# Kernel optimization log

Measured on AMD Instinct MI355X. Metric: run time of the kernel, lower is better.

The kernel has to match this reference:

```python
import jax, jax.numpy as jnp
import numpy as np

DEPTH, D, HEADS, PS, C_IN = 12, 1024, 8, 16, 1
B, H, W = 8, 512, 512


def setup_inputs() -> dict:
    key = jax.random.key(0)
    ks = jax.random.split(key, 8)
    s = 0.02
    rn = lambda k, shp: jax.random.normal(k, shp, jnp.float32) * s
    return dict(
        x=jax.random.normal(ks[0], (B, C_IN, H, W), jnp.float32),
        conv_w=rn(ks[1], (D, C_IN, PS, PS)),
        conv_b=jnp.zeros((D,), jnp.float32),
        ln1_g=jnp.ones((DEPTH, D), jnp.float32),
        ln1_b=jnp.zeros((DEPTH, D), jnp.float32),
        qkv_w=rn(ks[2], (DEPTH, 3 * D, D)),
        qkv_b=jnp.zeros((DEPTH, 3 * D), jnp.float32),
        proj_w=rn(ks[3], (DEPTH, D, D)),
        proj_b=jnp.zeros((DEPTH, D), jnp.float32),
        ln2_g=jnp.ones((DEPTH, D), jnp.float32),
        ln2_b=jnp.zeros((DEPTH, D), jnp.float32),
        fc1_w=rn(ks[4], (DEPTH, 2 * D, D)),
        fc1_b=jnp.zeros((DEPTH, 2 * D), jnp.float32),
        fc2_w=rn(ks[5], (DEPTH, D, 2 * D)),
        fc2_b=jnp.zeros((DEPTH, D), jnp.float32),
    )


def _layernorm(x, g, b, eps=1e-5):
    m = x.mean(-1, keepdims=True)
    v = ((x - m) ** 2).mean(-1, keepdims=True)
    return (x - m) * jax.lax.rsqrt(v + eps) * g + b


def _pos_encoding(n, d):
    # faithful to the source: angle = pos / 10000 ** (2*i/d) with i the EVEN index
    pos = jnp.arange(n, dtype=jnp.float32)[:, None]
    i_even = jnp.arange(0, d, 2, dtype=jnp.float32)
    ang = pos / (10000.0 ** (2.0 * i_even / d))
    return jnp.stack([jnp.sin(ang), jnp.cos(ang)], axis=-1).reshape(n, d)


def reference(x, conv_w, conv_b, ln1_g, ln1_b, qkv_w, qkv_b, proj_w, proj_b,
              ln2_g, ln2_b, fc1_w, fc1_b, fc2_w, fc2_b):
    b = x.shape[0]
    Hp, Wp = H // PS, W // PS
    n = Hp * Wp  # 1024 tokens
    hd = D // HEADS
    scale = float(hd) ** -0.5

    # patch embed: conv with stride == kernel  ==  per-patch matmul
    patches = x.reshape(b, C_IN, Hp, PS, Wp, PS).transpose(0, 2, 4, 1, 3, 5)
    patches = patches.reshape(b, n, C_IN * PS * PS)
    tok = patches @ conv_w.reshape(D, -1).T + conv_b
    tok = tok + _pos_encoding(n, D)

    def step(t, p):
        g1, b1, qw, qb, pw, pb, g2, b2, f1w, f1b, f2w, f2b = p
        h = _layernorm(t, g1, b1)
        qkv = (h @ qw.T + qb).reshape(b, n, 3, HEADS, hd).transpose(2, 0, 3, 1, 4)
        q, k, v = qkv[0], qkv[1], qkv[2]  # [b, heads, n, hd]
        att = jax.nn.softmax(jnp.einsum('bhqd,bhkd->bhqk', q, k) * scale, axis=-1)
        o = jnp.einsum('bhqk,bhkd->bhqd', att, v).transpose(0, 2, 1, 3).reshape(b, n, D)
        t = t + o @ pw.T + pb
        h = _layernorm(t, g2, b2)
        h = jax.nn.gelu(h @ f1w.T + f1b, approximate=False)
        t = t + h @ f2w.T + f2b
        return t, None

    tok, _ = jax.lax.scan(step, tok, (ln1_g, ln1_b, qkv_w, qkv_b, proj_w, proj_b,
                                      ln2_g, ln2_b, fc1_w, fc1_b, fc2_w, fc2_b))

    # reconstruction: tok -> (b, 4, ps*ps, Hp, Wp); scatter fina[:,:,i::ps,j::ps] = x[:,:,k]
    x4 = tok.reshape(b, n, D // 4, 4).transpose(0, 3, 2, 1).reshape(b, 4, PS, PS, Hp, Wp)
    fina = x4.transpose(0, 1, 4, 2, 5, 3).reshape(b, 4, H, W)  # fina[b,c,a*ps+i,bb*ps+j]
    # rearrange 'b (h w) p1 p2 -> b 1 (p1 h) (p2 w)' with h=w=2
    out = fina.reshape(b, 2, 2, H, W).transpose(0, 3, 1, 4, 2).reshape(b, 1, 2 * H, 2 * W)
    return out
```

## Files before the change

kernel.cpp:

```cpp
#include <hip/hip_runtime.h>
#include <hip/hip_bf16.h>
#include <stdint.h>

typedef unsigned short u16;
typedef __attribute__((ext_vector_type(8))) __bf16 bf16x8;
typedef __attribute__((ext_vector_type(4))) float  f32x4;

__device__ __forceinline__ float bf2f(u16 v) {
    union { unsigned int u; float f; } x; x.u = ((unsigned int)v) << 16; return x.f;
}
__device__ __forceinline__ u16 f2bf(float f) {
    union { float f; unsigned int u; } x; x.f = f;
    unsigned int u = x.u;
    unsigned int lsb = (u >> 16) & 1u;
    u += 0x7fffu + lsb;
    return (u16)(u >> 16);
}

#define GLDS16(gp, lp)                                                         \
    __builtin_amdgcn_global_load_lds(                                          \
        (const __attribute__((address_space(1))) void*)(gp),                   \
        (__attribute__((address_space(3))) void*)(lp), 16, 0, 0)

__global__ __launch_bounds__(256) void cvt_kernel(const float* __restrict__ src,
                                                  u16* __restrict__ dst, int n4)
{
    int gid = blockIdx.x * 256 + threadIdx.x;
    if (gid < n4) {
        float4 v = ((const float4*)src)[gid];
        ushort4 o;
        o.x = f2bf(v.x); o.y = f2bf(v.y); o.z = f2bf(v.z); o.w = f2bf(v.w);
        ((ushort4*)dst)[gid] = o;
    }
}

__global__ __launch_bounds__(256) void cvt4_kernel(
    const float* __restrict__ s0, const float* __restrict__ s1,
    const float* __restrict__ s2, const float* __restrict__ s3,
    u16* __restrict__ d0, u16* __restrict__ d1,
    u16* __restrict__ d2, u16* __restrict__ d3)
{
    int gid = blockIdx.x * 256 + threadIdx.x;
    const float* s; u16* d; int idx;
    if (gid < 786432)                { s = s0; d = d0; idx = gid; }
    else if (gid < 1048576)          { s = s1; d = d1; idx = gid - 786432; }
    else if (gid < 1572864)          { s = s2; d = d2; idx = gid - 1048576; }
    else                             { s = s3; d = d3; idx = gid - 1572864; }
    float4 v = ((const float4*)s)[idx];
    ushort4 o;
    o.x = f2bf(v.x); o.y = f2bf(v.y); o.z = f2bf(v.z); o.w = f2bf(v.w);
    ((ushort4*)d)[idx] = o;
}

__global__ __launch_bounds__(512, 2) void gemm8p(
    const u16* __restrict__ A, const u16* __restrict__ B,
    const float* __restrict__ bias, const float* __restrict__ res,
    void* __restrict__ Cout, int c_fp32,
    int K, int lda, int ldb, int ldc, int ldres, float scale, int act)
{
    __shared__ __align__(16) u16 As[4][128 * 32];
    __shared__ __align__(16) u16 Bs[4][256 * 32];

    int nt = K >> 5;

    int gx  = gridDim.x;
    int nwg = gx * gridDim.y;
    int bid = blockIdx.y * gx + blockIdx.x;
    int cpx = nwg >> 3;
    int swz = (bid & 7) * cpx + (bid >> 3);
    int m0 = (swz / gx) << 7;
    int n0 = (swz % gx) << 8;

    int t = threadIdx.x;
    int w = t >> 6, l = t & 63;
    int wm = w >> 2, wn = w & 3;
    int lg = l >> 4, lr = l & 15;

    int arow = t >> 2, aslot = t & 3;
    const u16* Ag  = A + (long long)(m0 + arow) * lda + ((aslot ^ ((arow >> 1) & 3)) << 3);
    const u16* Bg0 = B + (long long)(n0 + arow) * ldb + ((aslot ^ ((arow >> 1) & 3)) << 3);
    const u16* Bg1 = Bg0 + (long long)128 * ldb;

#define STAGE_A(tt)  GLDS16(Ag  + ((long long)(tt) << 5), &As[(tt) & 3][w << 9])
#define STAGE_B0(tt) GLDS16(Bg0 + ((long long)(tt) << 5), &Bs[(tt) & 3][w << 9])
#define STAGE_B1(tt) GLDS16(Bg1 + ((long long)(tt) << 5), &Bs[(tt) & 3][4096 + (w << 9)])

    int sx = lg ^ ((lr >> 1) & 3);
    const u16* Asr = &As[0][0] + (wm << 11) + (lr << 5) + (sx << 3);
    const u16* Bsr = &Bs[0][0] + (wn << 11) + (lr << 5) + (sx << 3);

    f32x4 acc[4][4];
#pragma unroll
    for (int i = 0; i < 4; i++)
#pragma unroll
        for (int j = 0; j < 4; j++)
            acc[i][j] = (f32x4){0.f, 0.f, 0.f, 0.f};

    STAGE_A(0); STAGE_B0(0); STAGE_B1(0);
    if (nt > 1) { STAGE_A(1); STAGE_B0(1); STAGE_B1(1); }
    if (nt > 2) { STAGE_A(2); STAGE_B0(2); STAGE_B1(2); }
    asm volatile("s_waitcnt vmcnt(6)" ::: "memory");
    __builtin_amdgcn_s_barrier();
    __builtin_amdgcn_sched_barrier(0);

    for (int tt = 0; tt < nt; ++tt) {
        int buf = tt & 3;
        const u16* Ab = Asr + (buf << 12);
        const u16* Bb = Bsr + (buf << 13);

        bf16x8 av[4], bv0[2];
#pragma unroll
        for (int i = 0; i < 4; i++) av[i]  = *(const bf16x8*)(Ab + i * 512);
#pragma unroll
        for (int j = 0; j < 2; j++) bv0[j] = *(const bf16x8*)(Bb + j * 512);
        if (tt + 3 < nt) { STAGE_A(tt + 3); STAGE_B0(tt + 3); }
        __builtin_amdgcn_s_barrier();
        __builtin_amdgcn_sched_barrier(0);
        __builtin_amdgcn_s_setprio(1);
#pragma unroll
        for (int j = 0; j < 2; j++)
#pragma unroll
            for (int i = 0; i < 4; i++)
                acc[i][j] = __builtin_amdgcn_mfma_f32_16x16x32_bf16(av[i], bv0[j], acc[i][j], 0, 0, 0);
        __builtin_amdgcn_s_setprio(0);
        __builtin_amdgcn_s_barrier();
        __builtin_amdgcn_sched_barrier(0);

        bf16x8 bv1[2];
#pragma unroll
        for (int j = 0; j < 2; j++) bv1[j] = *(const bf16x8*)(Bb + (2 + j) * 512);
        if (tt + 3 < nt) STAGE_B1(tt + 3);
        __builtin_amdgcn_s_barrier();
        __builtin_amdgcn_sched_barrier(0);
        __builtin_amdgcn_s_setprio(1);
#pragma unroll
        for (int j = 0; j < 2; j++)
#pragma unroll
            for (int i = 0; i < 4; i++)
                acc[i][2 + j] = __builtin_amdgcn_mfma_f32_16x16x32_bf16(av[i], bv1[j], acc[i][2 + j], 0, 0, 0);
        __builtin_amdgcn_s_setprio(0);
        if (tt < nt - 3)       asm volatile("s_waitcnt vmcnt(6)" ::: "memory");
        else if (tt == nt - 3) asm volatile("s_waitcnt vmcnt(3)" ::: "memory");
        else if (tt == nt - 2) asm volatile("s_waitcnt vmcnt(0)" ::: "memory");
        __builtin_amdgcn_s_barrier();
        __builtin_amdgcn_sched_barrier(0);
    }
#undef STAGE_A
#undef STAGE_B0
#undef STAGE_B1

    int rq = lg << 2;
#pragma unroll
    for (int j = 0; j < 4; j++) {
        int col = n0 + (wn << 6) + (j << 4) + lr;
        float bvv = bias ? bias[col] : 0.f;
#pragma unroll
        for (int i = 0; i < 4; i++) {
#pragma unroll
            for (int r = 0; r < 4; r++) {
                int row = m0 + (wm << 6) + (i << 4) + rq + r;
                float v = acc[i][j][r] * scale + bvv;
                if (act) v = 0.5f * v * (1.f + erff(v * 0.70710678118654752f));
                if (res) v += res[(long long)row * ldres + col];
                long long idx = (long long)row * ldc + col;
                if (c_fp32) ((float*)Cout)[idx] = v;
                else        ((u16*)Cout)[idx]  = f2bf(v);
            }
        }
    }
}

#define ASCALE 0.08838834764831845f

__global__ __launch_bounds__(256) void attn_kernel(
    const u16* __restrict__ qkv, const u16* __restrict__ vt,
    u16* __restrict__ out)
{
    __shared__ __align__(16) u16 Ks[64 * 128];
    __shared__ __align__(16) u16 Vs[128 * 64];
    __shared__ __align__(16) u16 Ps[4][32 * 72];

    int bh = blockIdx.y; int b = bh >> 3, hd = bh & 7;
    int q0 = blockIdx.x << 7;
    int t = threadIdx.x, w = t >> 6, l = t & 63;
    int lg = l >> 4, lr = l & 15;

    const u16* qp = qkv + ((long long)(b * 1024 + q0 + (w << 5) + lr)) * 3072
                        + hd * 128 + (lg << 3);
    bf16x8 qf[2][4];
#pragma unroll
    for (int rb = 0; rb < 2; rb++)
#pragma unroll
        for (int kf = 0; kf < 4; kf++)
            qf[rb][kf] = *(const bf16x8*)(qp + rb * 16 * 3072 + (kf << 5));

    const u16* kg = qkv + ((long long)(b * 1024)) * 3072 + 1024 + hd * 128;
    const u16* vg = vt + (long long)bh * 131072;
    u16* Pw = &Ps[w][0];

    f32x4 oa[2][8];
#pragma unroll
    for (int rb = 0; rb < 2; rb++)
#pragma unroll
        for (int db = 0; db < 8; db++)
            oa[rb][db] = (f32x4){0.f, 0.f, 0.f, 0.f};
    float m_run[2][4], l_run[2][4];
#pragma unroll
    for (int rb = 0; rb < 2; rb++)
#pragma unroll
        for (int r = 0; r < 4; r++) { m_run[rb][r] = -1e30f; l_run[rb][r] = 0.f; }

    for (int kv0 = 0; kv0 < 1024; kv0 += 64) {
#pragma unroll
        for (int i = 0; i < 4; i++) {
            int ck   = (((w << 2) + i) << 6) + l;
            int krow = ck >> 4;
            int kslot = (ck & 15) ^ (krow & 7);
            GLDS16(kg + (long long)(kv0 + krow) * 3072 + (kslot << 3),
                   Ks + (((w << 2) + i) << 9));
            int vd   = ck >> 3;
            int vslot = (ck & 7) ^ (vd & 7);
            GLDS16(vg + (long long)vd * 1024 + kv0 + (vslot << 3),
                   Vs + (((w << 2) + i) << 9));
        }
        __syncthreads();

        f32x4 s[2][4];
#pragma unroll
        for (int kb = 0; kb < 4; kb++) {
            s[0][kb] = (f32x4){0.f, 0.f, 0.f, 0.f};
            s[1][kb] = (f32x4){0.f, 0.f, 0.f, 0.f};
        }
#pragma unroll
        for (int kf = 0; kf < 4; kf++)
#pragma unroll
            for (int kb = 0; kb < 4; kb++) {
                bf16x8 bk = *(const bf16x8*)
                    &Ks[(((kb << 4) + lr) << 7) + (((((kf << 2) + lg)) ^ (lr & 7)) << 3)];
                s[0][kb] = __builtin_amdgcn_mfma_f32_16x16x32_bf16(qf[0][kf], bk, s[0][kb], 0, 0, 0);
                s[1][kb] = __builtin_amdgcn_mfma_f32_16x16x32_bf16(qf[1][kf], bk, s[1][kb], 0, 0, 0);
            }

#pragma unroll
        for (int rb = 0; rb < 2; rb++) {
            float mx[4], al[4], rs[4];
#pragma unroll
            for (int r = 0; r < 4; r++)
                mx[r] = fmaxf(fmaxf(s[rb][0][r], s[rb][1][r]),
                              fmaxf(s[rb][2][r], s[rb][3][r]));
#pragma unroll
            for (int mask = 1; mask < 16; mask <<= 1)
#pragma unroll
                for (int r = 0; r < 4; r++)
                    mx[r] = fmaxf(mx[r], __shfl_xor(mx[r], mask));
#pragma unroll
            for (int r = 0; r < 4; r++) {
                float mn = fmaxf(m_run[rb][r], mx[r] * ASCALE);
                al[r] = __expf(m_run[rb][r] - mn);
                m_run[rb][r] = mn;
                rs[r] = 0.f;
            }
#pragma unroll
            for (int kb = 0; kb < 4; kb++)
#pragma unroll
                for (int r = 0; r < 4; r++) {
                    float p = __expf(s[rb][kb][r] * ASCALE - m_run[rb][r]);
                    rs[r] += p;
                    Pw[((rb << 4) + (lg << 2) + r) * 72 + (kb << 4) + lr] = f2bf(p);
                }
#pragma unroll
            for (int mask = 1; mask < 16; mask <<= 1)
#pragma unroll
                for (int r = 0; r < 4; r++)
                    rs[r] += __shfl_xor(rs[r], mask);
#pragma unroll
            for (int r = 0; r < 4; r++)
                l_run[rb][r] = l_run[rb][r] * al[r] + rs[r];
#pragma unroll
            for (int db = 0; db < 8; db++)
#pragma unroll
                for (int r = 0; r < 4; r++)
                    oa[rb][db][r] *= al[r];
        }

#pragma unroll
        for (int ks = 0; ks < 2; ks++) {
            bf16x8 pa0 = *(const bf16x8*)&Pw[lr * 72 + (ks << 5) + (lg << 3)];
            bf16x8 pa1 = *(const bf16x8*)&Pw[(16 + lr) * 72 + (ks << 5) + (lg << 3)];
#pragma unroll
            for (int db = 0; db < 8; db++) {
                bf16x8 vf = *(const bf16x8*)
                    &Vs[(((db << 4) + lr) << 6) + ((((ks << 2) + lg) ^ (lr & 7)) << 3)];
                oa[0][db] = __builtin_amdgcn_mfma_f32_16x16x32_bf16(pa0, vf, oa[0][db], 0, 0, 0);
                oa[1][db] = __builtin_amdgcn_mfma_f32_16x16x32_bf16(pa1, vf, oa[1][db], 0, 0, 0);
            }
        }
        __syncthreads();
    }

    long long obase = ((long long)(b * 1024 + q0 + (w << 5)) << 10) + hd * 128;
#pragma unroll
    for (int rb = 0; rb < 2; rb++) {
        float il[4];
#pragma unroll
        for (int r = 0; r < 4; r++) il[r] = 1.f / l_run[rb][r];
#pragma unroll
        for (int db = 0; db < 8; db++)
#pragma unroll
            for (int r = 0; r < 4; r++)
                out[obase + (long long)((rb << 4) + (lg << 2) + r) * 1024
                          + (db << 4) + lr] = f2bf(oa[rb][db][r] * il[r]);
    }
}

__global__ __launch_bounds__(256) void patches_kernel(const float* __restrict__ x,
                                                      u16* __restrict__ p)
{
    int gid = blockIdx.x * 256 + threadIdx.x;
    int c = gid & 255, tk = gid >> 8;
    int b = tk >> 10, n = tk & 1023;
    int ph = n >> 5, pw = n & 31;
    int i = c >> 4, j = c & 15;
    p[gid] = f2bf(x[((long long)b << 18) + (long long)(ph * 16 + i) * 512 + pw * 16 + j]);
}

__global__ __launch_bounds__(256) void posenc_kernel(float* __restrict__ tok)
{
    int gid = blockIdx.x * 256 + threadIdx.x;
    int d = gid & 1023;
    int n = (gid >> 10) & 1023;
    int j = d >> 1;
    float ang = (float)n * exp2f(-13.287712379549449f * (float)j * (1.0f / 256.0f));
    float pe = (d & 1) ? cosf(ang) : sinf(ang);
    tok[gid] += pe;
}

__global__ __launch_bounds__(256) void ln_kernel(const float* __restrict__ x,
                                                 const float* __restrict__ g,
                                                 const float* __restrict__ b,
                                                 u16* __restrict__ y)
{
    int row = blockIdx.x, t = threadIdx.x;
    const float* xr = x + (long long)row * 1024;
    float v[4]; float s = 0.f, ss = 0.f;
#pragma unroll
    for (int i = 0; i < 4; i++) { v[i] = xr[i * 256 + t]; s += v[i]; ss += v[i] * v[i]; }
    __shared__ float rs[256], rss[256];
    rs[t] = s; rss[t] = ss; __syncthreads();
    for (int o = 128; o > 0; o >>= 1) {
        if (t < o) { rs[t] += rs[t + o]; rss[t] += rss[t + o]; }
        __syncthreads();
    }
    float mean = rs[0] * (1.f / 1024.f);
    float var  = rss[0] * (1.f / 1024.f) - mean * mean;
    float rstd = rsqrtf(var + 1e-5f);
    u16* yr = y + (long long)row * 1024;
#pragma unroll
    for (int i = 0; i < 4; i++) {
        int d = i * 256 + t;
        yr[d] = f2bf((v[i] - mean) * rstd * g[d] + b[d]);
    }
}

__global__ __launch_bounds__(256) void vt_kernel(const u16* __restrict__ qkv,
                                                 u16* __restrict__ vt)
{
    int bh   = blockIdx.x >> 4;
    int tile = blockIdx.x & 15;
    int b = bh >> 3, hd = bh & 7;
    int t = threadIdx.x;
    __shared__ u16 tl[64][130];
    int nk0 = tile * 64;
    int dcol = t & 127, r0 = t >> 7;
    const u16* src = qkv + ((long long)(b * 1024 + nk0)) * 3072 + 2048 + hd * 128 + dcol;
#pragma unroll
    for (int r = 0; r < 32; r++) {
        int nk = r0 + r * 2;
        tl[nk][dcol] = src[(long long)nk * 3072];
    }
    __syncthreads();
    u16* dst = vt + ((long long)bh * 128) * 1024 + nk0;
#pragma unroll
    for (int r = 0; r < 32; r++) {
        int flat = r * 256 + t;
        int d = flat >> 6, nk = flat & 63;
        dst[(long long)d * 1024 + nk] = tl[nk][d];
    }
}

__global__ __launch_bounds__(256) void recon_kernel(const float* __restrict__ tok,
                                                    float* __restrict__ out)
{
    int gid = blockIdx.x * 256 + threadIdx.x;
    int b  = gid >> 20;
    int y  = (gid >> 10) & 1023;
    int xx = gid & 1023;
    int p1 = y & 1,  hh = y >> 1,  a  = hh >> 4, i = hh & 15;
    int p2 = xx & 1, wv = xx >> 1, bb = wv >> 4, j = wv & 15;
    int n = a * 32 + bb;
    int d = ((i * 16 + j) << 2) + (p1 << 1) + p2;
    out[gid] = tok[((long long)(b * 1024 + n) << 10) + d];
}

extern "C" void kernel_launch(void* const* d_in, const int* in_sizes, int n_in,
                              void* d_out, int out_size, void* d_ws, size_t ws_size,
                              hipStream_t stream)
{
    (void)in_sizes; (void)n_in; (void)out_size; (void)ws_size;
    const float* x      = (const float*)d_in[0];
    const float* conv_w = (const float*)d_in[1];
    const float* conv_b = (const float*)d_in[2];
    const float* ln1_g  = (const float*)d_in[3];
    const float* ln1_b  = (const float*)d_in[4];
    const float* qkv_w  = (const float*)d_in[5];
    const float* qkv_b  = (const float*)d_in[6];
    const float* proj_w = (const float*)d_in[7];
    const float* proj_b = (const float*)d_in[8];
    const float* ln2_g  = (const float*)d_in[9];
    const float* ln2_b  = (const float*)d_in[10];
    const float* fc1_w  = (const float*)d_in[11];
    const float* fc1_b  = (const float*)d_in[12];
    const float* fc2_w  = (const float*)d_in[13];
    const float* fc2_b  = (const float*)d_in[14];

    char* ws = (char*)d_ws;
    float* tokf  = (float*)ws;
    u16* h       = (u16*)(ws + 33554432);
    u16* qkvb    = (u16*)(ws + 50331648);
    u16* vt      = (u16*)(ws + 100663296);
    u16* attnout = (u16*)(ws + 117440512);
    u16* mid     = (u16*)(ws + 134217728);
    u16* patches = (u16*)(ws + 167772160);
    u16* convw   = (u16*)(ws + 171966464);
    u16* wqkv    = (u16*)(ws + 172490752);
    u16* wproj   = (u16*)(ws + 178782208);
    u16* wfc1    = (u16*)(ws + 180879360);
    u16* wfc2    = (u16*)(ws + 185073664);

    dim3 blk(256);
    dim3 blk512(512);

    patches_kernel<<<dim3(8192), blk, 0, stream>>>(x, patches);
    cvt_kernel<<<dim3(256), blk, 0, stream>>>(conv_w, convw, 65536);
    gemm8p<<<dim3(4, 64), blk512, 0, stream>>>(
        patches, convw, conv_b, (const float*)nullptr, (void*)tokf, 1,
        256, 256, 256, 1024, 0, 1.0f, 0);
    posenc_kernel<<<dim3(32768), blk, 0, stream>>>(tokf);

    for (int L = 0; L < 12; L++) {
        cvt4_kernel<<<dim3(8192), blk, 0, stream>>>(
            qkv_w + (long long)L * 3145728, proj_w + (long long)L * 1048576,
            fc1_w + (long long)L * 2097152, fc2_w + (long long)L * 2097152,
            wqkv, wproj, wfc1, wfc2);

        ln_kernel<<<dim3(8192), blk, 0, stream>>>(
            tokf, ln1_g + L * 1024, ln1_b + L * 1024, h);

        gemm8p<<<dim3(12, 64), blk512, 0, stream>>>(
            h, wqkv, qkv_b + L * 3072, (const float*)nullptr, (void*)qkvb, 0,
            1024, 1024, 1024, 3072, 0, 1.0f, 0);

        vt_kernel<<<dim3(1024), blk, 0, stream>>>(qkvb, vt);

        attn_kernel<<<dim3(8, 64, 1), blk, 0, stream>>>(qkvb, vt, attnout);

        gemm8p<<<dim3(4, 64), blk512, 0, stream>>>(
            attnout, wproj, proj_b + L * 1024, tokf, (void*)tokf, 1,
            1024, 1024, 1024, 1024, 1024, 1.0f, 0);

        ln_kernel<<<dim3(8192), blk, 0, stream>>>(
            tokf, ln2_g + L * 1024, ln2_b + L * 1024, h);

        gemm8p<<<dim3(8, 64), blk512, 0, stream>>>(
            h, wfc1, fc1_b + L * 2048, (const float*)nullptr, (void*)mid, 0,
            1024, 1024, 1024, 2048, 0, 1.0f, 1);

        gemm8p<<<dim3(4, 64), blk512, 0, stream>>>(
            mid, wfc2, fc2_b + L * 1024, tokf, (void*)tokf, 1,
            2048, 2048, 2048, 1024, 1024, 1.0f, 0);
    }

    recon_kernel<<<dim3(32768), blk, 0, stream>>>(tokf, (float*)d_out);
}
```

Baseline: 4.915 ms.

## Enlarge GEMM tile to 256x256 with BK=64 double-buffered LDS pipeline

```diff
diff --git a/kernel.cpp b/kernel.cpp
--- a/kernel.cpp
+++ b/kernel.cpp
@@ -58,108 +58,158 @@
     void* __restrict__ Cout, int c_fp32,
     int K, int lda, int ldb, int ldc, int ldres, float scale, int act)
 {
-    __shared__ __align__(16) u16 As[4][128 * 32];
-    __shared__ __align__(16) u16 Bs[4][256 * 32];
-
-    int nt = K >> 5;
+    __shared__ __align__(16) u16 As[2][256 * 64];
+    __shared__ __align__(16) u16 Bs[2][256 * 64];
+
+    int nt = K >> 6;
 
     int gx  = gridDim.x;
     int nwg = gx * gridDim.y;
     int bid = blockIdx.y * gx + blockIdx.x;
     int cpx = nwg >> 3;
     int swz = (bid & 7) * cpx + (bid >> 3);
-    int m0 = (swz / gx) << 7;
+    int m0 = (swz / gx) << 8;
     int n0 = (swz % gx) << 8;
 
     int t = threadIdx.x;
     int w = t >> 6, l = t & 63;
     int wm = w >> 2, wn = w & 3;
-    int lg = l >> 4, lr = l & 15;
-
-    int arow = t >> 2, aslot = t & 3;
-    const u16* Ag  = A + (long long)(m0 + arow) * lda + ((aslot ^ ((arow >> 1) & 3)) << 3);
-    const u16* Bg0 = B + (long long)(n0 + arow) * ldb + ((aslot ^ ((arow >> 1) & 3)) << 3);
-    const u16* Bg1 = Bg0 + (long long)128 * ldb;
-
-#define STAGE_A(tt)  GLDS16(Ag  + ((long long)(tt) << 5), &As[(tt) & 3][w << 9])
-#define STAGE_B0(tt) GLDS16(Bg0 + ((long long)(tt) << 5), &Bs[(tt) & 3][w << 9])
-#define STAGE_B1(tt) GLDS16(Bg1 + ((long long)(tt) << 5), &Bs[(tt) & 3][4096 + (w << 9)])
-
-    int sx = lg ^ ((lr >> 1) & 3);
-    const u16* Asr = &As[0][0] + (wm << 11) + (lr << 5) + (sx << 3);
-    const u16* Bsr = &Bs[0][0] + (wn << 11) + (lr << 5) + (sx << 3);
-
-    f32x4 acc[4][4];
-#pragma unroll
-    for (int i = 0; i < 4; i++)
-#pragma unroll
-        for (int j = 0; j < 4; j++)
-            acc[i][j] = (f32x4){0.f, 0.f, 0.f, 0.f};
-
-    STAGE_A(0); STAGE_B0(0); STAGE_B1(0);
-    if (nt > 1) { STAGE_A(1); STAGE_B0(1); STAGE_B1(1); }
-    if (nt > 2) { STAGE_A(2); STAGE_B0(2); STAGE_B1(2); }
+    int lg = l >> 4, lr = l & 15, r7 = lr & 7;
+
+    int tr = t >> 3, ts = t & 7;
+    int tsw = ts ^ (tr & 7);
+    const u16* Ag = A + (long long)(m0 + tr) * lda + (tsw << 3);
+    const u16* Bg = B + (long long)(n0 + tr) * ldb + (tsw << 3);
+    long long a64 = (long long)lda << 6, a128 = (long long)lda << 7;
+    long long b64 = (long long)ldb << 6, b128 = (long long)ldb << 7;
+
+    u16* AsW = &As[0][0] + (w << 9);
+    u16* BsW = &Bs[0][0] + (w << 9);
+
+#define SG_A0(tt) { u16* d_ = AsW + (((tt) & 1) << 14);                        \
+        const u16* g_ = Ag + ((long long)(tt) << 6);                           \
+        GLDS16(g_, d_); GLDS16(g_ + a64, d_ + 4096); }
+#define SG_A1(tt) { u16* d_ = AsW + (((tt) & 1) << 14) + 8192;                 \
+        const u16* g_ = Ag + ((long long)(tt) << 6) + a128;                    \
+        GLDS16(g_, d_); GLDS16(g_ + a64, d_ + 4096); }
+#define SG_B0(tt) { u16* d_ = BsW + (((tt) & 1) << 14);                        \
+        const u16* g_ = Bg + ((long long)(tt) << 6);                           \
+        GLDS16(g_, d_); GLDS16(g_ + b64, d_ + 4096); }
+#define SG_B1(tt) { u16* d_ = BsW + (((tt) & 1) << 14) + 8192;                 \
+        const u16* g_ = Bg + ((long long)(tt) << 6) + b128;                    \
+        GLDS16(g_, d_); GLDS16(g_ + b64, d_ + 4096); }
+
+    int aoff0 = ((wm << 7) + lr) * 64 + ((lg ^ r7) << 3);
+    int aoff1 = ((wm << 7) + lr) * 64 + (((4 | lg) ^ r7) << 3);
+    int boff0 = ((wn << 6) + lr) * 64 + ((lg ^ r7) << 3);
+    int boff1 = ((wn << 6) + lr) * 64 + (((4 | lg) ^ r7) << 3);
+
+    f32x4 acc[8][4];
+#pragma unroll
+    for (int m = 0; m < 8; m++)
+#pragma unroll
+        for (int n = 0; n < 4; n++)
+            acc[m][n] = (f32x4){0.f, 0.f, 0.f, 0.f};
+
+    SG_A0(0); SG_A1(0); SG_B0(0); SG_B1(0);
+    SG_A0(1); SG_B0(1); SG_B1(1);
     asm volatile("s_waitcnt vmcnt(6)" ::: "memory");
     __builtin_amdgcn_s_barrier();
     __builtin_amdgcn_sched_barrier(0);
 
     for (int tt = 0; tt < nt; ++tt) {
-        int buf = tt & 3;
-        const u16* Ab = Asr + (buf << 12);
-        const u16* Bb = Bsr + (buf << 13);
-
-        bf16x8 av[4], bv0[2];
-#pragma unroll
-        for (int i = 0; i < 4; i++) av[i]  = *(const bf16x8*)(Ab + i * 512);
-#pragma unroll
-        for (int j = 0; j < 2; j++) bv0[j] = *(const bf16x8*)(Bb + j * 512);
-        if (tt + 3 < nt) { STAGE_A(tt + 3); STAGE_B0(tt + 3); }
-        __builtin_amdgcn_s_barrier();
+        const u16* Ab = &As[0][0] + ((tt & 1) << 14);
+        const u16* Bb = &Bs[0][0] + ((tt & 1) << 14);
+        bf16x8 a[4], bb0[4], bb1[4];
+
+#pragma unroll
+        for (int i = 0; i < 4; i++) a[i]   = *(const bf16x8*)(Ab + aoff0 + i * 1024);
+#pragma unroll
+        for (int n = 0; n < 4; n++) bb0[n] = *(const bf16x8*)(Bb + boff0 + n * 1024);
+        if (tt + 1 < nt) SG_A1(tt + 1);
+        __builtin_amdgcn_sched_barrier(0);
+        __builtin_amdgcn_s_barrier();
+        asm volatile("s_waitcnt lgkmcnt(0)" ::: "memory");
         __builtin_amdgcn_sched_barrier(0);
         __builtin_amdgcn_s_setprio(1);
 #pragma unroll
-        for (int j = 0; j < 2; j++)
+        for (int n = 0; n < 4; n++)
 #pragma unroll
             for (int i = 0; i < 4; i++)
-                acc[i][j] = __builtin_amdgcn_mfma_f32_16x16x32_bf16(av[i], bv0[j], acc[i][j], 0, 0, 0);
+                acc[i][n] = __builtin_amdgcn_mfma_f32_16x16x32_bf16(a[i], bb0[n], acc[i][n], 0, 0, 0);
         __builtin_amdgcn_s_setprio(0);
         __builtin_amdgcn_s_barrier();
         __builtin_amdgcn_sched_barrier(0);
 
-        bf16x8 bv1[2];
-#pragma unroll
-        for (int j = 0; j < 2; j++) bv1[j] = *(const bf16x8*)(Bb + (2 + j) * 512);
-        if (tt + 3 < nt) STAGE_B1(tt + 3);
-        __builtin_amdgcn_s_barrier();
+#pragma unroll
+        for (int i = 0; i < 4; i++) a[i] = *(const bf16x8*)(Ab + aoff0 + 4096 + i * 1024);
+        __builtin_amdgcn_sched_barrier(0);
+        __builtin_amdgcn_s_barrier();
+        asm volatile("s_waitcnt lgkmcnt(0)" ::: "memory");
         __builtin_amdgcn_sched_barrier(0);
         __builtin_amdgcn_s_setprio(1);
 #pragma unroll
-        for (int j = 0; j < 2; j++)
+        for (int n = 0; n < 4; n++)
 #pragma unroll
             for (int i = 0; i < 4; i++)
-                acc[i][2 + j] = __builtin_amdgcn_mfma_f32_16x16x32_bf16(av[i], bv1[j], acc[i][2 + j], 0, 0, 0);
+                acc[4 + i][n] = __builtin_amdgcn_mfma_f32_16x16x32_bf16(a[i], bb0[n], acc[4 + i][n], 0, 0, 0);
         __builtin_amdgcn_s_setprio(0);
-        if (tt < nt - 3)       asm volatile("s_waitcnt vmcnt(6)" ::: "memory");
-        else if (tt == nt - 3) asm volatile("s_waitcnt vmcnt(3)" ::: "memory");
-        else if (tt == nt - 2) asm volatile("s_waitcnt vmcnt(0)" ::: "memory");
-        __builtin_amdgcn_s_barrier();
-        __builtin_amdgcn_sched_barrier(0);
-    }
-#undef STAGE_A
-#undef STAGE_B0
-#undef STAGE_B1
+        __builtin_amdgcn_s_barrier();
+        __builtin_amdgcn_sched_barrier(0);
+
+#pragma unroll
+        for (int i = 0; i < 4; i++) a[i]   = *(const bf16x8*)(Ab + aoff1 + i * 1024);
+#pragma unroll
+        for (int n = 0; n < 4; n++) bb1[n] = *(const bf16x8*)(Bb + boff1 + n * 1024);
+        __builtin_amdgcn_sched_barrier(0);
+        __builtin_amdgcn_s_barrier();
+        asm volatile("s_waitcnt lgkmcnt(0)" ::: "memory");
+        __builtin_amdgcn_sched_barrier(0);
+        __builtin_amdgcn_s_setprio(1);
+#pragma unroll
+        for (int n = 0; n < 4; n++)
+#pragma unroll
+            for (int i = 0; i < 4; i++)
+                acc[i][n] = __builtin_amdgcn_mfma_f32_16x16x32_bf16(a[i], bb1[n], acc[i][n], 0, 0, 0);
+        __builtin_amdgcn_s_setprio(0);
+        __builtin_amdgcn_s_barrier();
+        __builtin_amdgcn_sched_barrier(0);
+
+#pragma unroll
+        for (int i = 0; i < 4; i++) a[i] = *(const bf16x8*)(Ab + aoff1 + 4096 + i * 1024);
+        if (tt + 2 < nt) { SG_A0(tt + 2); SG_B0(tt + 2); SG_B1(tt + 2); }
+        __builtin_amdgcn_sched_barrier(0);
+        __builtin_amdgcn_s_barrier();
+        asm volatile("s_waitcnt lgkmcnt(0)" ::: "memory");
+        __builtin_amdgcn_sched_barrier(0);
+        __builtin_amdgcn_s_setprio(1);
+#pragma unroll
+        for (int n = 0; n < 4; n++)
+#pragma unroll
+            for (int i = 0; i < 4; i++)
+                acc[4 + i][n] = __builtin_amdgcn_mfma_f32_16x16x32_bf16(a[i], bb1[n], acc[4 + i][n], 0, 0, 0);
+        __builtin_amdgcn_s_setprio(0);
+        if (tt + 2 < nt)      { asm volatile("s_waitcnt vmcnt(6)" ::: "memory"); }
+        else if (tt + 1 < nt) { asm volatile("s_waitcnt vmcnt(0)" ::: "memory"); }
+        __builtin_amdgcn_s_barrier();
+        __builtin_amdgcn_sched_barrier(0);
+    }
+#undef SG_A0
+#undef SG_A1
+#undef SG_B0
+#undef SG_B1
 
     int rq = lg << 2;
 #pragma unroll
-    for (int j = 0; j < 4; j++) {
-        int col = n0 + (wn << 6) + (j << 4) + lr;
+    for (int n = 0; n < 4; n++) {
+        int col = n0 + (wn << 6) + (n << 4) + lr;
         float bvv = bias ? bias[col] : 0.f;
 #pragma unroll
-        for (int i = 0; i < 4; i++) {
+        for (int m = 0; m < 8; m++) {
 #pragma unroll
             for (int r = 0; r < 4; r++) {
-                int row = m0 + (wm << 6) + (i << 4) + rq + r;
-                float v = acc[i][j][r] * scale + bvv;
+                int row = m0 + (wm << 7) + (m << 4) + rq + r;
+                float v = acc[m][n][r] * scale + bvv;
                 if (act) v = 0.5f * v * (1.f + erff(v * 0.70710678118654752f));
                 if (res) v += res[(long long)row * ldres + col];
                 long long idx = (long long)row * ldc + col;
@@ -442,7 +492,7 @@
 
     patches_kernel<<<dim3(8192), blk, 0, stream>>>(x, patches);
     cvt_kernel<<<dim3(256), blk, 0, stream>>>(conv_w, convw, 65536);
-    gemm8p<<<dim3(4, 64), blk512, 0, stream>>>(
+    gemm8p<<<dim3(4, 32), blk512, 0, stream>>>(
         patches, convw, conv_b, (const float*)nullptr, (void*)tokf, 1,
         256, 256, 256, 1024, 0, 1.0f, 0);
     posenc_kernel<<<dim3(32768), blk, 0, stream>>>(tokf);
@@ -456,7 +506,7 @@
         ln_kernel<<<dim3(8192), blk, 0, stream>>>(
             tokf, ln1_g + L * 1024, ln1_b + L * 1024, h);
 
-        gemm8p<<<dim3(12, 64), blk512, 0, stream>>>(
+        gemm8p<<<dim3(12, 32), blk512, 0, stream>>>(
             h, wqkv, qkv_b + L * 3072, (const float*)nullptr, (void*)qkvb, 0,
             1024, 1024, 1024, 3072, 0, 1.0f, 0);
 
@@ -464,18 +514,18 @@
 
         attn_kernel<<<dim3(8, 64, 1), blk, 0, stream>>>(qkvb, vt, attnout);
 
-        gemm8p<<<dim3(4, 64), blk512, 0, stream>>>(
+        gemm8p<<<dim3(4, 32), blk512, 0, stream>>>(
             attnout, wproj, proj_b + L * 1024, tokf, (void*)tokf, 1,
             1024, 1024, 1024, 1024, 1024, 1.0f, 0);
 
         ln_kernel<<<dim3(8192), blk, 0, stream>>>(
             tokf, ln2_g + L * 1024, ln2_b + L * 1024, h);
 
-        gemm8p<<<dim3(8, 64), blk512, 0, stream>>>(
+        gemm8p<<<dim3(8, 32), blk512, 0, stream>>>(
             h, wfc1, fc1_b + L * 2048, (const float*)nullptr, (void*)mid, 0,
             1024, 1024, 1024, 2048, 0, 1.0f, 1);
 
-        gemm8p<<<dim3(4, 64), blk512, 0, stream>>>(
+        gemm8p<<<dim3(4, 32), blk512, 0, stream>>>(
             mid, wfc2, fc2_b + L * 1024, tokf, (void*)tokf, 1,
             2048, 2048, 2048, 1024, 1024, 1.0f, 0);
     }
```

Result: slower. 5.526 ms (+12.4%).

## Switch GEMM to 3-stage LDS pipeline with single barrier per k-step

Applied to the files above, without the earlier changes.

```diff
diff --git a/kernel.cpp b/kernel.cpp
--- a/kernel.cpp
+++ b/kernel.cpp
@@ -52,14 +52,14 @@
     ((ushort4*)d)[idx] = o;
 }
 
-__global__ __launch_bounds__(512, 2) void gemm8p(
+__global__ __launch_bounds__(512, 4) void gemm3b(
     const u16* __restrict__ A, const u16* __restrict__ B,
     const float* __restrict__ bias, const float* __restrict__ res,
     void* __restrict__ Cout, int c_fp32,
     int K, int lda, int ldb, int ldc, int ldres, float scale, int act)
 {
-    __shared__ __align__(16) u16 As[4][128 * 32];
-    __shared__ __align__(16) u16 Bs[4][256 * 32];
+    __shared__ __align__(16) u16 As[3][128 * 32];
+    __shared__ __align__(16) u16 Bs[3][256 * 32];
 
     int nt = K >> 5;
 
@@ -77,13 +77,15 @@
     int lg = l >> 4, lr = l & 15;
 
     int arow = t >> 2, aslot = t & 3;
-    const u16* Ag  = A + (long long)(m0 + arow) * lda + ((aslot ^ ((arow >> 1) & 3)) << 3);
-    const u16* Bg0 = B + (long long)(n0 + arow) * ldb + ((aslot ^ ((arow >> 1) & 3)) << 3);
-    const u16* Bg1 = Bg0 + (long long)128 * ldb;
-
-#define STAGE_A(tt)  GLDS16(Ag  + ((long long)(tt) << 5), &As[(tt) & 3][w << 9])
-#define STAGE_B0(tt) GLDS16(Bg0 + ((long long)(tt) << 5), &Bs[(tt) & 3][w << 9])
-#define STAGE_B1(tt) GLDS16(Bg1 + ((long long)(tt) << 5), &Bs[(tt) & 3][4096 + (w << 9)])
+    int asw  = aslot ^ ((arow >> 1) & 3);
+    const u16* Ag  = A + (long long)(m0 + arow) * lda + (asw << 3);
+    const u16* Bg0 = B + (long long)(n0 + arow) * ldb + (asw << 3);
+    const u16* Bg1 = Bg0 + ((long long)ldb << 7);
+
+#define SG(tt, bb) {                                                           \
+        GLDS16(Ag  + ((long long)(tt) << 5), &As[bb][w << 9]);                 \
+        GLDS16(Bg0 + ((long long)(tt) << 5), &Bs[bb][w << 9]);                 \
+        GLDS16(Bg1 + ((long long)(tt) << 5), &Bs[bb][4096 + (w << 9)]); }
 
     int sx = lg ^ ((lr >> 1) & 3);
     const u16* Asr = &As[0][0] + (wm << 11) + (lr << 5) + (sx << 3);
@@ -96,58 +98,40 @@
         for (int j = 0; j < 4; j++)
             acc[i][j] = (f32x4){0.f, 0.f, 0.f, 0.f};
 
-    STAGE_A(0); STAGE_B0(0); STAGE_B1(0);
-    if (nt > 1) { STAGE_A(1); STAGE_B0(1); STAGE_B1(1); }
-    if (nt > 2) { STAGE_A(2); STAGE_B0(2); STAGE_B1(2); }
-    asm volatile("s_waitcnt vmcnt(6)" ::: "memory");
+    SG(0, 0); SG(1, 1);
+    asm volatile("s_waitcnt vmcnt(3)" ::: "memory");
     __builtin_amdgcn_s_barrier();
     __builtin_amdgcn_sched_barrier(0);
 
+    int bufR = 0;
     for (int tt = 0; tt < nt; ++tt) {
-        int buf = tt & 3;
-        const u16* Ab = Asr + (buf << 12);
-        const u16* Bb = Bsr + (buf << 13);
-
-        bf16x8 av[4], bv0[2];
-#pragma unroll
-        for (int i = 0; i < 4; i++) av[i]  = *(const bf16x8*)(Ab + i * 512);
-#pragma unroll
-        for (int j = 0; j < 2; j++) bv0[j] = *(const bf16x8*)(Bb + j * 512);
-        if (tt + 3 < nt) { STAGE_A(tt + 3); STAGE_B0(tt + 3); }
+        const u16* Ab = Asr + (bufR << 12);
+        const u16* Bb = Bsr + (bufR << 13);
+
+        bf16x8 av[4], bv[4];
+#pragma unroll
+        for (int i = 0; i < 4; i++) av[i] = *(const bf16x8*)(Ab + i * 512);
+#pragma unroll
+        for (int j = 0; j < 4; j++) bv[j] = *(const bf16x8*)(Bb + j * 512);
+
+        if (tt + 2 < nt) {
+            int bw = bufR == 0 ? 2 : bufR - 1;
+            SG(tt + 2, bw);
+        }
+
+#pragma unroll
+        for (int i = 0; i < 4; i++)
+#pragma unroll
+            for (int j = 0; j < 4; j++)
+                acc[i][j] = __builtin_amdgcn_mfma_f32_16x16x32_bf16(av[i], bv[j], acc[i][j], 0, 0, 0);
+
+        if (tt + 2 < nt)      { asm volatile("s_waitcnt vmcnt(3)" ::: "memory"); }
+        else if (tt + 1 < nt) { asm volatile("s_waitcnt vmcnt(0)" ::: "memory"); }
         __builtin_amdgcn_s_barrier();
         __builtin_amdgcn_sched_barrier(0);
-        __builtin_amdgcn_s_setprio(1);
-#pragma unroll
-        for (int j = 0; j < 2; j++)
-#pragma unroll
-            for (int i = 0; i < 4; i++)
-                acc[i][j] = __builtin_amdgcn_mfma_f32_16x16x32_bf16(av[i], bv0[j], acc[i][j], 0, 0, 0);
-        __builtin_amdgcn_s_setprio(0);
-        __builtin_amdgcn_s_barrier();
-        __builtin_amdgcn_sched_barrier(0);
-
-        bf16x8 bv1[2];
-#pragma unroll
-        for (int j = 0; j < 2; j++) bv1[j] = *(const bf16x8*)(Bb + (2 + j) * 512);
-        if (tt + 3 < nt) STAGE_B1(tt + 3);
-        __builtin_amdgcn_s_barrier();
-        __builtin_amdgcn_sched_barrier(0);
-        __builtin_amdgcn_s_setprio(1);
-#pragma unroll
-        for (int j = 0; j < 2; j++)
-#pragma unroll
-            for (int i = 0; i < 4; i++)
-                acc[i][2 + j] = __builtin_amdgcn_mfma_f32_16x16x32_bf16(av[i], bv1[j], acc[i][2 + j], 0, 0, 0);
-        __builtin_amdgcn_s_setprio(0);
-        if (tt < nt - 3)       asm volatile("s_waitcnt vmcnt(6)" ::: "memory");
-        else if (tt == nt - 3) asm volatile("s_waitcnt vmcnt(3)" ::: "memory");
-        else if (tt == nt - 2) asm volatile("s_waitcnt vmcnt(0)" ::: "memory");
-        __builtin_amdgcn_s_barrier();
-        __builtin_amdgcn_sched_barrier(0);
-    }
-#undef STAGE_A
-#undef STAGE_B0
-#undef STAGE_B1
+        bufR = bufR == 2 ? 0 : bufR + 1;
+    }
+#undef SG
 
     int rq = lg << 2;
 #pragma unroll
@@ -442,7 +426,7 @@
 
     patches_kernel<<<dim3(8192), blk, 0, stream>>>(x, patches);
     cvt_kernel<<<dim3(256), blk, 0, stream>>>(conv_w, convw, 65536);
-    gemm8p<<<dim3(4, 64), blk512, 0, stream>>>(
+    gemm3b<<<dim3(4, 64), blk512, 0, stream>>>(
         patches, convw, conv_b, (const float*)nullptr, (void*)tokf, 1,
         256, 256, 256, 1024, 0, 1.0f, 0);
     posenc_kernel<<<dim3(32768), blk, 0, stream>>>(tokf);
@@ -456,7 +440,7 @@
         ln_kernel<<<dim3(8192), blk, 0, stream>>>(
             tokf, ln1_g + L * 1024, ln1_b + L * 1024, h);
 
-        gemm8p<<<dim3(12, 64), blk512, 0, stream>>>(
+        gemm3b<<<dim3(12, 64), blk512, 0, stream>>>(
             h, wqkv, qkv_b + L * 3072, (const float*)nullptr, (void*)qkvb, 0,
             1024, 1024, 1024, 3072, 0, 1.0f, 0);
 
@@ -464,18 +448,18 @@
 
         attn_kernel<<<dim3(8, 64, 1), blk, 0, stream>>>(qkvb, vt, attnout);
 
-        gemm8p<<<dim3(4, 64), blk512, 0, stream>>>(
+        gemm3b<<<dim3(4, 64), blk512, 0, stream>>>(
             attnout, wproj, proj_b + L * 1024, tokf, (void*)tokf, 1,
             1024, 1024, 1024, 1024, 1024, 1.0f, 0);
 
         ln_kernel<<<dim3(8192), blk, 0, stream>>>(
             tokf, ln2_g + L * 1024, ln2_b + L * 1024, h);
 
-        gemm8p<<<dim3(8, 64), blk512, 0, stream>>>(
+        gemm3b<<<dim3(8, 64), blk512, 0, stream>>>(
             h, wfc1, fc1_b + L * 2048, (const float*)nullptr, (void*)mid, 0,
             1024, 1024, 1024, 2048, 0, 1.0f, 1);
 
-        gemm8p<<<dim3(4, 64), blk512, 0, stream>>>(
+        gemm3b<<<dim3(4, 64), blk512, 0, stream>>>(
             mid, wfc2, fc2_b + L * 1024, tokf, (void*)tokf, 1,
             2048, 2048, 2048, 1024, 1024, 1.0f, 0);
     }
```

Result: faster. 4.451 ms (-9.4%).
